# Kernel optimization log

Hardware: AMD Instinct MI355X
Metric: run time of the kernel (lower is better)

## Reference

```python
import jax, jax.numpy as jnp
import numpy as np

SEQ_LEN, BATCH, TAGS = 512, 1024, 32
START_IDX, END_IDX = 30, 31
NEG = -10000.0


def setup_inputs() -> dict:
    key = jax.random.key(0)
    k1, k2 = jax.random.split(key)
    feats = jax.random.normal(k1, (SEQ_LEN, BATCH, TAGS), dtype=jnp.float32)
    mask = jnp.ones((SEQ_LEN, BATCH), dtype=jnp.float32)
    # xavier-normal-ish transition, then apply START/END constraints as in reset_parameters
    transition = jax.random.normal(k2, (TAGS, TAGS), dtype=jnp.float32) * (2.0 / (TAGS + TAGS)) ** 0.5
    transition = transition.at[START_IDX, :].set(NEG)
    transition = transition.at[:, END_IDX].set(NEG)
    return {"feats": feats, "mask": mask, "transition": transition}


def reference(feats, mask, transition):
    # feats: (T, N, M), mask: (T, N), transition: (M, M)
    batch_size, tag_size = feats.shape[1], feats.shape[2]
    alpha0 = jnp.full((batch_size, tag_size), NEG, dtype=feats.dtype)
    alpha0 = alpha0.at[:, START_IDX].set(0.0)

    def step(alpha, inp):
        feat_t, mask_t = inp  # (N, M), (N,)
        # score[n, j, i] = alpha[n, i] + transition[j, i] + feat[n, j]
        score = alpha[:, None, :] + transition[None, :, :] + feat_t[:, :, None]
        new_alpha = jax.nn.logsumexp(score, axis=-1)  # (N, M)
        m = mask_t[:, None]
        alpha = new_alpha * m + alpha * (1.0 - m)
        return alpha, None

    alpha, _ = jax.lax.scan(step, alpha0, (feats, mask))
    alpha = alpha + transition[END_IDX][None, :]
    return jax.nn.logsumexp(alpha, axis=-1)  # (N,)
```

## Files before the change

### kernel.cpp

```cpp
#include <hip/hip_runtime.h>


constexpr int SEQ = 512, BATCH = 1024, TAGS = 32;
constexpr int BPB = 8;
constexpr int CH = 8;
constexpr int NCH = (SEQ / 2) / CH;
constexpr int RINGN = 4;
constexpr int SSTRIDE = BPB * TAGS;
constexpr int FSLOT = CH * SSTRIDE;
constexpr int MSLOT = CH * BPB;

#define LOG2E 1.4426950408889634f
#define LN2   0.6931471805599453f

typedef __attribute__((ext_vector_type(8))) short short8;
typedef __attribute__((ext_vector_type(4))) float float4v;
union Frag8 { unsigned u[4]; short8 v; };

__device__ __forceinline__ unsigned pk_rn(float x, float y) {
  return __builtin_amdgcn_perm(__float_as_uint(y) + 0x8000u,
                               __float_as_uint(x) + 0x8000u, 0x07060302u);
}
__device__ __forceinline__ unsigned pk_tr(float x, float y) {
  return __builtin_amdgcn_perm(__float_as_uint(y), __float_as_uint(x), 0x07060302u);
}

__device__ __forceinline__ void gld16(const float* g, float* l) {
  __builtin_amdgcn_global_load_lds((const __attribute__((address_space(1))) void*)g,
                                   (__attribute__((address_space(3))) void*)l, 16, 0, 0);
}
__device__ __forceinline__ void gld4(const float* g, float* l) {
  __builtin_amdgcn_global_load_lds((const __attribute__((address_space(1))) void*)g,
                                   (__attribute__((address_space(3))) void*)l, 4, 0, 0);
}

template <bool FWD>
__device__ __forceinline__ void produce(
    const float* __restrict__ feats, const float* __restrict__ maskp,
    float* __restrict__ FFd, float* __restrict__ MMd, int b0, int lane) {
  const int bs = lane >> 3;
  const int tg = 4 * ((lane & 7) ^ (bs & 7));
  const size_t t0 = FWD ? 0 : (size_t)(SEQ - 1);
  const float* gF0 = feats + t0 * BATCH * TAGS + (size_t)(b0 + bs) * TAGS + tg;
  const float* gM0 = maskp +
      (FWD ? (size_t)(lane >> 3) : (size_t)(SEQ - 1 - (lane >> 3))) * BATCH +
      b0 + (lane & 7);
  const ptrdiff_t fstep = FWD ? (ptrdiff_t)(BATCH * TAGS) : -(ptrdiff_t)(BATCH * TAGS);
  const ptrdiff_t mstep = FWD ? (ptrdiff_t)BATCH : -(ptrdiff_t)BATCH;

  auto FILL = [&](int k) {
    float* fb = FFd + (k & (RINGN - 1)) * FSLOT;
    float* mb = MMd + (k & (RINGN - 1)) * MSLOT;
#pragma unroll
    for (int j = 0; j < CH; ++j)
      gld16(gF0 + (ptrdiff_t)(CH * k + j) * fstep, fb + j * SSTRIDE);
    gld4(gM0 + (ptrdiff_t)(CH * k) * mstep, mb);
  };

  FILL(0); FILL(1); FILL(2);
  asm volatile("s_waitcnt vmcnt(18)" ::: "memory");
  __builtin_amdgcn_s_barrier();
  for (int k = 0; k < NCH; ++k) {
    if (k < NCH - 3) {
      FILL(k + 3);
      asm volatile("s_waitcnt vmcnt(18)" ::: "memory");
    } else if (k == NCH - 3) {
      asm volatile("s_waitcnt vmcnt(9)" ::: "memory");
    } else if (k == NCH - 2) {
      asm volatile("s_waitcnt vmcnt(0)" ::: "memory");
    }
    __builtin_amdgcn_s_barrier();
  }
  __syncthreads();
}

template <bool FWD>
__device__ __forceinline__ void consume(
    const float* __restrict__ trans, float* __restrict__ out,
    const float* __restrict__ FFd, const float* __restrict__ MMd,
    float* __restrict__ vbuf, float* __restrict__ c2buf, int b0, int lane) {
  const int s = lane & 15, q = lane >> 4;

  int sig[8];
#pragma unroll
  for (int i = 0; i < 8; ++i) sig[i] = (i < 4) ? (4 * q + i) : (16 + 4 * q + (i - 4));
  Frag8 e0, e1;
#pragma unroll
  for (int p = 0; p < 4; ++p) {
    if (FWD) {
      e0.u[p] = pk_rn(__builtin_amdgcn_exp2f(trans[s * TAGS + sig[2 * p]] * LOG2E),
                      __builtin_amdgcn_exp2f(trans[s * TAGS + sig[2 * p + 1]] * LOG2E));
      e1.u[p] = pk_rn(__builtin_amdgcn_exp2f(trans[(16 + s) * TAGS + sig[2 * p]] * LOG2E),
                      __builtin_amdgcn_exp2f(trans[(16 + s) * TAGS + sig[2 * p + 1]] * LOG2E));
    } else {
      e0.u[p] = pk_rn(__builtin_amdgcn_exp2f(trans[sig[2 * p] * TAGS + s] * LOG2E),
                      __builtin_amdgcn_exp2f(trans[sig[2 * p + 1] * TAGS + s] * LOG2E));
      e1.u[p] = pk_rn(__builtin_amdgcn_exp2f(trans[sig[2 * p] * TAGS + 16 + s] * LOG2E),
                      __builtin_amdgcn_exp2f(trans[sig[2 * p + 1] * TAGS + 16 + s] * LOG2E));
    }
  }

  float a[8];
#pragma unroll
  for (int i = 0; i < 8; ++i) {
    if (FWD) a[i] = (q == 3 && i == 6) ? 1.0f : 0.0f;
    else a[i] = __builtin_amdgcn_exp2f(
        trans[31 * TAGS + ((i < 4) ? (4 * q + i) : (16 + 4 * q + (i - 4)))] * LOG2E);
  }
  Frag8 Bf;
  Bf.u[0] = pk_tr(a[0], a[1]); Bf.u[1] = pk_tr(a[2], a[3]);
  Bf.u[2] = pk_tr(a[4], a[5]); Bf.u[3] = pk_tr(a[6], a[7]);
  float c2 = 0.f;
  const float4v zerov = {0.f, 0.f, 0.f, 0.f};

  const int off0 = s * 32 + ((q ^ (s & 7)) << 2);
  const int off1 = s * 32 + (((q + 4) ^ (s & 7)) << 2);

  float4v rA0, rA1, rB0, rB1;
  float mAv, mBv;
  float4v Fc0, Fc1;
  float mc;

  __builtin_amdgcn_s_barrier();
  __builtin_amdgcn_sched_barrier(0);
  rA0 = *(const float4v*)(FFd + 0 * SSTRIDE + off0);
  rA1 = *(const float4v*)(FFd + 0 * SSTRIDE + off1);
  mAv = MMd[0 * BPB + (s & 7)];
  rB0 = *(const float4v*)(FFd + 1 * SSTRIDE + off0);
  rB1 = *(const float4v*)(FFd + 1 * SSTRIDE + off1);
  mBv = MMd[1 * BPB + (s & 7)];
#pragma unroll
  for (int i = 0; i < 4; ++i) {
    Fc0[i] = __builtin_amdgcn_exp2f(rA0[i] * LOG2E);
    Fc1[i] = __builtin_amdgcn_exp2f(rA1[i] * LOG2E);
  }
  mc = mAv;

  for (int k = 0; k < NCH; ++k) {
    const float* fb = FFd + (k & (RINGN - 1)) * FSLOT;
    const float* mb = MMd + (k & (RINGN - 1)) * MSLOT;
#pragma unroll
    for (int j = 0; j < CH; ++j) {
      if (j < CH - 2) {
        float4v& c0 = (j & 1) ? rB0 : rA0;
        float4v& c1 = (j & 1) ? rB1 : rA1;
        float& cmv = (j & 1) ? mBv : mAv;
        c0 = *(const float4v*)(fb + (j + 2) * SSTRIDE + off0);
        c1 = *(const float4v*)(fb + (j + 2) * SSTRIDE + off1);
        cmv = mb[(j + 2) * BPB + (s & 7)];
      }

      const bool mv = (mc != 0.0f);
      if (FWD) {
        const float4v D0 = __builtin_amdgcn_mfma_f32_16x16x32_bf16(e0.v, Bf.v, zerov, 0, 0, 0);
        const float4v D1 = __builtin_amdgcn_mfma_f32_16x16x32_bf16(e1.v, Bf.v, zerov, 0, 0, 0);
#pragma unroll
        for (int i = 0; i < 4; ++i) {
          a[i] = mv ? D0[i] * Fc0[i] : a[i];
          a[4 + i] = mv ? D1[i] * Fc1[i] : a[4 + i];
        }
      } else {
        float tb[8];
#pragma unroll
        for (int i = 0; i < 4; ++i) { tb[i] = a[i] * Fc0[i]; tb[4 + i] = a[4 + i] * Fc1[i]; }
        Frag8 Bp;
        Bp.u[0] = pk_tr(tb[0], tb[1]); Bp.u[1] = pk_tr(tb[2], tb[3]);
        Bp.u[2] = pk_tr(tb[4], tb[5]); Bp.u[3] = pk_tr(tb[6], tb[7]);
        const float4v D0 = __builtin_amdgcn_mfma_f32_16x16x32_bf16(e0.v, Bp.v, zerov, 0, 0, 0);
        const float4v D1 = __builtin_amdgcn_mfma_f32_16x16x32_bf16(e1.v, Bp.v, zerov, 0, 0, 0);
#pragma unroll
        for (int i = 0; i < 4; ++i) {
          a[i] = mv ? D0[i] : a[i];
          a[4 + i] = mv ? D1[i] : a[4 + i];
        }
      }
      if (j == CH - 1) {
        float mx = fmaxf(fmaxf(fmaxf(a[0], a[1]), fmaxf(a[2], a[3])),
                         fmaxf(fmaxf(a[4], a[5]), fmaxf(a[6], a[7])));
        mx = fmaxf(mx, __shfl_xor(mx, 16, 64));
        mx = fmaxf(mx, __shfl_xor(mx, 32, 64));
        const int ex = (int)((__float_as_uint(mx) >> 23) & 0xFFu) - 127;
        const float scl = __uint_as_float((unsigned)(127 - ex) << 23);
#pragma unroll
        for (int i = 0; i < 8; ++i) a[i] *= scl;
        c2 += (float)ex;
      }
      if (FWD) {
        Bf.u[0] = pk_tr(a[0], a[1]); Bf.u[1] = pk_tr(a[2], a[3]);
        Bf.u[2] = pk_tr(a[4], a[5]); Bf.u[3] = pk_tr(a[6], a[7]);
      }

      if (j < CH - 1) {
        const float4v& n0 = (j & 1) ? rA0 : rB0;
        const float4v& n1 = (j & 1) ? rA1 : rB1;
        const float nm = (j & 1) ? mAv : mBv;
#pragma unroll
        for (int i = 0; i < 4; ++i) {
          Fc0[i] = __builtin_amdgcn_exp2f(n0[i] * LOG2E);
          Fc1[i] = __builtin_amdgcn_exp2f(n1[i] * LOG2E);
        }
        mc = nm;
      }
    }
    asm volatile("s_waitcnt lgkmcnt(0)" ::: "memory");
    __builtin_amdgcn_s_barrier();
    __builtin_amdgcn_sched_barrier(0);
    if (k < NCH - 1) {
      const float* fn = FFd + ((k + 1) & (RINGN - 1)) * FSLOT;
      const float* mn = MMd + ((k + 1) & (RINGN - 1)) * MSLOT;
      rA0 = *(const float4v*)(fn + 0 * SSTRIDE + off0);
      rA1 = *(const float4v*)(fn + 0 * SSTRIDE + off1);
      mAv = mn[0 * BPB + (s & 7)];
      rB0 = *(const float4v*)(fn + 1 * SSTRIDE + off0);
      rB1 = *(const float4v*)(fn + 1 * SSTRIDE + off1);
      mBv = mn[1 * BPB + (s & 7)];
#pragma unroll
      for (int i = 0; i < 4; ++i) {
        Fc0[i] = __builtin_amdgcn_exp2f(rA0[i] * LOG2E);
        Fc1[i] = __builtin_amdgcn_exp2f(rA1[i] * LOG2E);
      }
      mc = mAv;
    }
  }

  if (!FWD) {
    float4v lo = {a[0], a[1], a[2], a[3]}, hi = {a[4], a[5], a[6], a[7]};
    *(float4v*)(vbuf + lane * 8) = lo;
    *(float4v*)(vbuf + lane * 8 + 4) = hi;
    if (lane < 8) c2buf[lane] = c2;
  }
  __syncthreads();
  if (FWD) {
    const float4v v0 = *(const float4v*)(vbuf + lane * 8);
    const float4v v1 = *(const float4v*)(vbuf + lane * 8 + 4);
    float dot = a[0] * v0[0] + a[1] * v0[1] + a[2] * v0[2] + a[3] * v0[3] +
                a[4] * v1[0] + a[5] * v1[1] + a[6] * v1[2] + a[7] * v1[3];
    dot += __shfl_xor(dot, 16, 64);
    dot += __shfl_xor(dot, 32, 64);
    if (lane < 8)
      out[b0 + lane] = LN2 * (c2 + c2buf[lane] + __builtin_amdgcn_logf(dot));
  }
}

extern "C" __global__ void __launch_bounds__(256, 1) crf_scan(
    const float* __restrict__ feats, const float* __restrict__ mask,
    const float* __restrict__ trans, float* __restrict__ out) {
  __shared__ float FF[2][RINGN][FSLOT];
  __shared__ float MM[2][RINGN][MSLOT];
  __shared__ float vbuf[512];
  __shared__ float c2buf[16];
  const int wid = threadIdx.x >> 6;
  const int lane = threadIdx.x & 63;
  const int b0 = blockIdx.x * BPB;

  if (wid == 0)
    consume<true>(trans, out, &FF[0][0][0], &MM[0][0][0], vbuf, c2buf, b0, lane);
  else if (wid == 1)
    consume<false>(trans, out, &FF[1][0][0], &MM[1][0][0], vbuf, c2buf, b0, lane);
  else if (wid == 2)
    produce<true>(feats, mask, &FF[0][0][0], &MM[0][0][0], b0, lane);
  else
    produce<false>(feats, mask, &FF[1][0][0], &MM[1][0][0], b0, lane);
}

extern "C" void kernel_launch(void* const* d_in, const int* in_sizes, int n_in,
                              void* d_out, int out_size, void* d_ws, size_t ws_size,
                              hipStream_t stream) {
  const float* feats = (const float*)d_in[0];
  const float* mask  = (const float*)d_in[1];
  const float* trans = (const float*)d_in[2];
  float* out = (float*)d_out;
  hipLaunchKernelGGL(crf_scan, dim3(BATCH / BPB), dim3(256), 0, stream,
                     feats, mask, trans, out);
}
```

Baseline: 119.8 us.

## Move feature exp into producer waves and add all-valid mask fast path

Producer waves now load features into registers, compute exp2 of them, and write the exponentiated values to LDS. Previously they used direct global-to-LDS copies, and the consumers computed the exponentials on their serial critical path. Producers also compute a per-chunk flag that is set when every mask value is nonzero. Consumers use it to skip the per-step mask reads and selects. The LDS ring is shrunk from four slots to two, which leaves less prefetch slack and adds register-staged loads in the producers.

```diff
diff --git a/kernel.cpp b/kernel.cpp
--- a/kernel.cpp
+++ b/kernel.cpp
@@ -5,7 +5,7 @@
 constexpr int BPB = 8;
 constexpr int CH = 8;
 constexpr int NCH = (SEQ / 2) / CH;
-constexpr int RINGN = 4;
+constexpr int RINGN = 2;
 constexpr int SSTRIDE = BPB * TAGS;
 constexpr int FSLOT = CH * SSTRIDE;
 constexpr int MSLOT = CH * BPB;
@@ -25,59 +25,68 @@
   return __builtin_amdgcn_perm(__float_as_uint(y), __float_as_uint(x), 0x07060302u);
 }
 
-__device__ __forceinline__ void gld16(const float* g, float* l) {
-  __builtin_amdgcn_global_load_lds((const __attribute__((address_space(1))) void*)g,
-                                   (__attribute__((address_space(3))) void*)l, 16, 0, 0);
-}
-__device__ __forceinline__ void gld4(const float* g, float* l) {
-  __builtin_amdgcn_global_load_lds((const __attribute__((address_space(1))) void*)g,
-                                   (__attribute__((address_space(3))) void*)l, 4, 0, 0);
-}
-
 template <bool FWD>
 __device__ __forceinline__ void produce(
     const float* __restrict__ feats, const float* __restrict__ maskp,
-    float* __restrict__ FFd, float* __restrict__ MMd, int b0, int lane) {
-  const int bs = lane >> 3;
-  const int tg = 4 * ((lane & 7) ^ (bs & 7));
-  const size_t t0 = FWD ? 0 : (size_t)(SEQ - 1);
-  const float* gF0 = feats + t0 * BATCH * TAGS + (size_t)(b0 + bs) * TAGS + tg;
-  const float* gM0 = maskp +
-      (FWD ? (size_t)(lane >> 3) : (size_t)(SEQ - 1 - (lane >> 3))) * BATCH +
-      b0 + (lane & 7);
+    float* __restrict__ FFd, float* __restrict__ MMd,
+    unsigned* __restrict__ FLGd, int b0, int lane) {
+  const int bl = lane >> 3;
+  const int tgd = (lane & 7) * 4;
+  const size_t t0off = FWD ? 0 : (size_t)(SEQ - 1) * BATCH * TAGS;
+  const float* gF = feats + t0off + (size_t)(b0 + bl) * TAGS + tgd;
+  const float* gM = maskp + b0 + (lane & 7) + (FWD ? 0 : (size_t)(SEQ - 1) * BATCH);
   const ptrdiff_t fstep = FWD ? (ptrdiff_t)(BATCH * TAGS) : -(ptrdiff_t)(BATCH * TAGS);
   const ptrdiff_t mstep = FWD ? (ptrdiff_t)BATCH : -(ptrdiff_t)BATCH;
-
-  auto FILL = [&](int k) {
-    float* fb = FFd + (k & (RINGN - 1)) * FSLOT;
-    float* mb = MMd + (k & (RINGN - 1)) * MSLOT;
-#pragma unroll
-    for (int j = 0; j < CH; ++j)
-      gld16(gF0 + (ptrdiff_t)(CH * k + j) * fstep, fb + j * SSTRIDE);
-    gld4(gM0 + (ptrdiff_t)(CH * k) * mstep, mb);
-  };
-
-  FILL(0); FILL(1); FILL(2);
-  asm volatile("s_waitcnt vmcnt(18)" ::: "memory");
+  const int wd = bl * 32 + (((lane & 7) ^ (bl & 7)) << 2);
+
+  float4v SA[CH], SB[CH];
+  float mA, mB;
+
+#define LOADC(S, MV, c)                                                       \
+  { _Pragma("unroll") for (int j = 0; j < CH; ++j)                            \
+      S[j] = *(const float4v*)(gF + (ptrdiff_t)(CH * (c) + j) * fstep);       \
+    MV = gM[(ptrdiff_t)(CH * (c) + (lane >> 3)) * mstep]; }
+
+#define PROC(S, MV, c)                                                        \
+  { float* fb = FFd + ((c) & (RINGN - 1)) * FSLOT;                            \
+    float* mb = MMd + ((c) & (RINGN - 1)) * MSLOT;                            \
+    const unsigned flag = (__ballot(MV != 0.0f) == ~0ull) ? 1u : 0u;          \
+    _Pragma("unroll") for (int j = 0; j < CH; ++j) {                          \
+      float4v e;                                                              \
+      _Pragma("unroll") for (int i = 0; i < 4; ++i)                           \
+        e[i] = __builtin_amdgcn_exp2f(S[j][i] * LOG2E);                       \
+      *(float4v*)(fb + j * SSTRIDE + wd) = e;                                 \
+    }                                                                         \
+    mb[lane] = MV;                                                            \
+    if (lane == 0) FLGd[(c) & (RINGN - 1)] = flag; }
+
+  LOADC(SA, mA, 0)
+  LOADC(SB, mB, 1)
+  PROC(SA, mA, 0)
+  asm volatile("s_waitcnt lgkmcnt(0)" ::: "memory");
   __builtin_amdgcn_s_barrier();
+#pragma unroll 2
   for (int k = 0; k < NCH; ++k) {
-    if (k < NCH - 3) {
-      FILL(k + 3);
-      asm volatile("s_waitcnt vmcnt(18)" ::: "memory");
-    } else if (k == NCH - 3) {
-      asm volatile("s_waitcnt vmcnt(9)" ::: "memory");
-    } else if (k == NCH - 2) {
-      asm volatile("s_waitcnt vmcnt(0)" ::: "memory");
-    }
+    if ((k & 1) == 0) {
+      if (k + 2 < NCH) LOADC(SA, mA, k + 2)
+      if (k + 1 < NCH) PROC(SB, mB, k + 1)
+    } else {
+      if (k + 2 < NCH) LOADC(SB, mB, k + 2)
+      if (k + 1 < NCH) PROC(SA, mA, k + 1)
+    }
+    asm volatile("s_waitcnt lgkmcnt(0)" ::: "memory");
     __builtin_amdgcn_s_barrier();
   }
   __syncthreads();
+#undef LOADC
+#undef PROC
 }
 
 template <bool FWD>
 __device__ __forceinline__ void consume(
     const float* __restrict__ trans, float* __restrict__ out,
     const float* __restrict__ FFd, const float* __restrict__ MMd,
+    const unsigned* __restrict__ FLGd,
     float* __restrict__ vbuf, float* __restrict__ c2buf, int b0, int lane) {
   const int s = lane & 15, q = lane >> 4;
 
@@ -117,89 +126,96 @@
   const int off1 = s * 32 + (((q + 4) ^ (s & 7)) << 2);
 
   float4v rA0, rA1, rB0, rB1;
-  float mAv, mBv;
-  float4v Fc0, Fc1;
-  float mc;
 
   __builtin_amdgcn_s_barrier();
   __builtin_amdgcn_sched_barrier(0);
   rA0 = *(const float4v*)(FFd + 0 * SSTRIDE + off0);
   rA1 = *(const float4v*)(FFd + 0 * SSTRIDE + off1);
-  mAv = MMd[0 * BPB + (s & 7)];
   rB0 = *(const float4v*)(FFd + 1 * SSTRIDE + off0);
   rB1 = *(const float4v*)(FFd + 1 * SSTRIDE + off1);
-  mBv = MMd[1 * BPB + (s & 7)];
-#pragma unroll
-  for (int i = 0; i < 4; ++i) {
-    Fc0[i] = __builtin_amdgcn_exp2f(rA0[i] * LOG2E);
-    Fc1[i] = __builtin_amdgcn_exp2f(rA1[i] * LOG2E);
-  }
-  mc = mAv;
+
+#define RENORM_A()                                                            \
+  { float mx = fmaxf(fmaxf(fmaxf(a[0], a[1]), fmaxf(a[2], a[3])),             \
+                     fmaxf(fmaxf(a[4], a[5]), fmaxf(a[6], a[7])));            \
+    mx = fmaxf(mx, __shfl_xor(mx, 16, 64));                                   \
+    mx = fmaxf(mx, __shfl_xor(mx, 32, 64));                                   \
+    const int ex = (int)((__float_as_uint(mx) >> 23) & 0xFFu) - 127;          \
+    const float scl = __uint_as_float((unsigned)(127 - ex) << 23);            \
+    _Pragma("unroll") for (int i = 0; i < 8; ++i) a[i] *= scl;                \
+    c2 += (float)ex; }
 
   for (int k = 0; k < NCH; ++k) {
     const float* fb = FFd + (k & (RINGN - 1)) * FSLOT;
     const float* mb = MMd + (k & (RINGN - 1)) * MSLOT;
-#pragma unroll
-    for (int j = 0; j < CH; ++j) {
-      if (j < CH - 2) {
-        float4v& c0 = (j & 1) ? rB0 : rA0;
-        float4v& c1 = (j & 1) ? rB1 : rA1;
-        float& cmv = (j & 1) ? mBv : mAv;
-        c0 = *(const float4v*)(fb + (j + 2) * SSTRIDE + off0);
-        c1 = *(const float4v*)(fb + (j + 2) * SSTRIDE + off1);
-        cmv = mb[(j + 2) * BPB + (s & 7)];
+    const unsigned fl = __builtin_amdgcn_readfirstlane(FLGd[k & (RINGN - 1)]);
+    if (fl) {
+#pragma unroll
+      for (int j = 0; j < CH; ++j) {
+        const float4v F0 = (j & 1) ? rB0 : rA0;
+        const float4v F1 = (j & 1) ? rB1 : rA1;
+        if (FWD) {
+          const float4v D0 = __builtin_amdgcn_mfma_f32_16x16x32_bf16(e0.v, Bf.v, zerov, 0, 0, 0);
+          const float4v D1 = __builtin_amdgcn_mfma_f32_16x16x32_bf16(e1.v, Bf.v, zerov, 0, 0, 0);
+#pragma unroll
+          for (int i = 0; i < 4; ++i) { a[i] = D0[i] * F0[i]; a[4 + i] = D1[i] * F1[i]; }
+          if (j == CH - 1) RENORM_A()
+          Bf.u[0] = pk_tr(a[0], a[1]); Bf.u[1] = pk_tr(a[2], a[3]);
+          Bf.u[2] = pk_tr(a[4], a[5]); Bf.u[3] = pk_tr(a[6], a[7]);
+        } else {
+          float tb[8];
+#pragma unroll
+          for (int i = 0; i < 4; ++i) { tb[i] = a[i] * F0[i]; tb[4 + i] = a[4 + i] * F1[i]; }
+          Frag8 Bp;
+          Bp.u[0] = pk_tr(tb[0], tb[1]); Bp.u[1] = pk_tr(tb[2], tb[3]);
+          Bp.u[2] = pk_tr(tb[4], tb[5]); Bp.u[3] = pk_tr(tb[6], tb[7]);
+          const float4v D0 = __builtin_amdgcn_mfma_f32_16x16x32_bf16(e0.v, Bp.v, zerov, 0, 0, 0);
+          const float4v D1 = __builtin_amdgcn_mfma_f32_16x16x32_bf16(e1.v, Bp.v, zerov, 0, 0, 0);
+#pragma unroll
+          for (int i = 0; i < 4; ++i) { a[i] = D0[i]; a[4 + i] = D1[i]; }
+          if (j == CH - 1) RENORM_A()
+        }
+        if (j < CH - 2) {
+          ((j & 1) ? rB0 : rA0) = *(const float4v*)(fb + (j + 2) * SSTRIDE + off0);
+          ((j & 1) ? rB1 : rA1) = *(const float4v*)(fb + (j + 2) * SSTRIDE + off1);
+        }
       }
-
-      const bool mv = (mc != 0.0f);
-      if (FWD) {
-        const float4v D0 = __builtin_amdgcn_mfma_f32_16x16x32_bf16(e0.v, Bf.v, zerov, 0, 0, 0);
-        const float4v D1 = __builtin_amdgcn_mfma_f32_16x16x32_bf16(e1.v, Bf.v, zerov, 0, 0, 0);
-#pragma unroll
-        for (int i = 0; i < 4; ++i) {
-          a[i] = mv ? D0[i] * Fc0[i] : a[i];
-          a[4 + i] = mv ? D1[i] * Fc1[i] : a[4 + i];
-        }
-      } else {
-        float tb[8];
-#pragma unroll
-        for (int i = 0; i < 4; ++i) { tb[i] = a[i] * Fc0[i]; tb[4 + i] = a[4 + i] * Fc1[i]; }
-        Frag8 Bp;
-        Bp.u[0] = pk_tr(tb[0], tb[1]); Bp.u[1] = pk_tr(tb[2], tb[3]);
-        Bp.u[2] = pk_tr(tb[4], tb[5]); Bp.u[3] = pk_tr(tb[6], tb[7]);
-        const float4v D0 = __builtin_amdgcn_mfma_f32_16x16x32_bf16(e0.v, Bp.v, zerov, 0, 0, 0);
-        const float4v D1 = __builtin_amdgcn_mfma_f32_16x16x32_bf16(e1.v, Bp.v, zerov, 0, 0, 0);
-#pragma unroll
-        for (int i = 0; i < 4; ++i) {
-          a[i] = mv ? D0[i] : a[i];
-          a[4 + i] = mv ? D1[i] : a[4 + i];
-        }
-      }
-      if (j == CH - 1) {
-        float mx = fmaxf(fmaxf(fmaxf(a[0], a[1]), fmaxf(a[2], a[3])),
-                         fmaxf(fmaxf(a[4], a[5]), fmaxf(a[6], a[7])));
-        mx = fmaxf(mx, __shfl_xor(mx, 16, 64));
-        mx = fmaxf(mx, __shfl_xor(mx, 32, 64));
-        const int ex = (int)((__float_as_uint(mx) >> 23) & 0xFFu) - 127;
-        const float scl = __uint_as_float((unsigned)(127 - ex) << 23);
-#pragma unroll
-        for (int i = 0; i < 8; ++i) a[i] *= scl;
-        c2 += (float)ex;
-      }
-      if (FWD) {
-        Bf.u[0] = pk_tr(a[0], a[1]); Bf.u[1] = pk_tr(a[2], a[3]);
-        Bf.u[2] = pk_tr(a[4], a[5]); Bf.u[3] = pk_tr(a[6], a[7]);
-      }
-
-      if (j < CH - 1) {
-        const float4v& n0 = (j & 1) ? rA0 : rB0;
-        const float4v& n1 = (j & 1) ? rA1 : rB1;
-        const float nm = (j & 1) ? mAv : mBv;
-#pragma unroll
-        for (int i = 0; i < 4; ++i) {
-          Fc0[i] = __builtin_amdgcn_exp2f(n0[i] * LOG2E);
-          Fc1[i] = __builtin_amdgcn_exp2f(n1[i] * LOG2E);
-        }
-        mc = nm;
+    } else {
+#pragma unroll
+      for (int j = 0; j < CH; ++j) {
+        const float4v F0 = (j & 1) ? rB0 : rA0;
+        const float4v F1 = (j & 1) ? rB1 : rA1;
+        const bool mv = (mb[j * BPB + (s & 7)] != 0.0f);
+        if (FWD) {
+          const float4v D0 = __builtin_amdgcn_mfma_f32_16x16x32_bf16(e0.v, Bf.v, zerov, 0, 0, 0);
+          const float4v D1 = __builtin_amdgcn_mfma_f32_16x16x32_bf16(e1.v, Bf.v, zerov, 0, 0, 0);
+#pragma unroll
+          for (int i = 0; i < 4; ++i) {
+            a[i] = mv ? D0[i] * F0[i] : a[i];
+            a[4 + i] = mv ? D1[i] * F1[i] : a[4 + i];
+          }
+          if (j == CH - 1) RENORM_A()
+          Bf.u[0] = pk_tr(a[0], a[1]); Bf.u[1] = pk_tr(a[2], a[3]);
+          Bf.u[2] = pk_tr(a[4], a[5]); Bf.u[3] = pk_tr(a[6], a[7]);
+        } else {
+          float tb[8];
+#pragma unroll
+          for (int i = 0; i < 4; ++i) { tb[i] = a[i] * F0[i]; tb[4 + i] = a[4 + i] * F1[i]; }
+          Frag8 Bp;
+          Bp.u[0] = pk_tr(tb[0], tb[1]); Bp.u[1] = pk_tr(tb[2], tb[3]);
+          Bp.u[2] = pk_tr(tb[4], tb[5]); Bp.u[3] = pk_tr(tb[6], tb[7]);
+          const float4v D0 = __builtin_amdgcn_mfma_f32_16x16x32_bf16(e0.v, Bp.v, zerov, 0, 0, 0);
+          const float4v D1 = __builtin_amdgcn_mfma_f32_16x16x32_bf16(e1.v, Bp.v, zerov, 0, 0, 0);
+#pragma unroll
+          for (int i = 0; i < 4; ++i) {
+            a[i] = mv ? D0[i] : a[i];
+            a[4 + i] = mv ? D1[i] : a[4 + i];
+          }
+          if (j == CH - 1) RENORM_A()
+        }
+        if (j < CH - 2) {
+          ((j & 1) ? rB0 : rA0) = *(const float4v*)(fb + (j + 2) * SSTRIDE + off0);
+          ((j & 1) ? rB1 : rA1) = *(const float4v*)(fb + (j + 2) * SSTRIDE + off1);
+        }
       }
     }
     asm volatile("s_waitcnt lgkmcnt(0)" ::: "memory");
@@ -207,21 +223,13 @@
     __builtin_amdgcn_sched_barrier(0);
     if (k < NCH - 1) {
       const float* fn = FFd + ((k + 1) & (RINGN - 1)) * FSLOT;
-      const float* mn = MMd + ((k + 1) & (RINGN - 1)) * MSLOT;
       rA0 = *(const float4v*)(fn + 0 * SSTRIDE + off0);
       rA1 = *(const float4v*)(fn + 0 * SSTRIDE + off1);
-      mAv = mn[0 * BPB + (s & 7)];
       rB0 = *(const float4v*)(fn + 1 * SSTRIDE + off0);
       rB1 = *(const float4v*)(fn + 1 * SSTRIDE + off1);
-      mBv = mn[1 * BPB + (s & 7)];
-#pragma unroll
-      for (int i = 0; i < 4; ++i) {
-        Fc0[i] = __builtin_amdgcn_exp2f(rA0[i] * LOG2E);
-        Fc1[i] = __builtin_amdgcn_exp2f(rA1[i] * LOG2E);
-      }
-      mc = mAv;
-    }
-  }
+    }
+  }
+#undef RENORM_A
 
   if (!FWD) {
     float4v lo = {a[0], a[1], a[2], a[3]}, hi = {a[4], a[5], a[6], a[7]};
@@ -247,6 +255,7 @@
     const float* __restrict__ trans, float* __restrict__ out) {
   __shared__ float FF[2][RINGN][FSLOT];
   __shared__ float MM[2][RINGN][MSLOT];
+  __shared__ unsigned FLG[2][RINGN];
   __shared__ float vbuf[512];
   __shared__ float c2buf[16];
   const int wid = threadIdx.x >> 6;
@@ -254,13 +263,13 @@
   const int b0 = blockIdx.x * BPB;
 
   if (wid == 0)
-    consume<true>(trans, out, &FF[0][0][0], &MM[0][0][0], vbuf, c2buf, b0, lane);
+    consume<true>(trans, out, &FF[0][0][0], &MM[0][0][0], &FLG[0][0], vbuf, c2buf, b0, lane);
   else if (wid == 1)
-    consume<false>(trans, out, &FF[1][0][0], &MM[1][0][0], vbuf, c2buf, b0, lane);
+    consume<false>(trans, out, &FF[1][0][0], &MM[1][0][0], &FLG[1][0], vbuf, c2buf, b0, lane);
   else if (wid == 2)
-    produce<true>(feats, mask, &FF[0][0][0], &MM[0][0][0], b0, lane);
+    produce<true>(feats, mask, &FF[0][0][0], &MM[0][0][0], &FLG[0][0], b0, lane);
   else
-    produce<false>(feats, mask, &FF[1][0][0], &MM[1][0][0], b0, lane);
+    produce<false>(feats, mask, &FF[1][0][0], &MM[1][0][0], &FLG[1][0], b0, lane);
 }
 
 extern "C" void kernel_launch(void* const* d_in, const int* in_sizes, int n_in,
```

New measurement: 106.9 us. -10.8%, faster.
